# Performance work log

Hardware: AMD Instinct MI355X
Metric: run time of the kernel (lower is better)

Reference implementation:

```python
import jax, jax.numpy as jnp
import numpy as np

B, C, H, W = 4, 512, 96, 96
NH = 8
HD = C // NH
NC = 128
D = 768
L = H * W
EPS = 1e-5  # torch LayerNorm default


def _l2n(x, axis):
    # F.normalize: x / max(||x||, 1e-12)
    return x / jnp.maximum(jnp.linalg.norm(x, axis=axis, keepdims=True), 1e-12)


def _ln2d(x, g, b):
    # LayerNorm2d: normalize over channel dim of (B,C,H,W)
    mu = x.mean(1, keepdims=True)
    var = ((x - mu) ** 2).mean(1, keepdims=True)
    return (x - mu) / jnp.sqrt(var + EPS) * g[None, :, None, None] + b[None, :, None, None]


def _conv1x1(x, w):
    return jnp.einsum('oc,bchw->bohw', w, x)


def setup_inputs() -> dict:
    key = jax.random.key(0)
    ks = jax.random.split(key, 9)
    s = 0.02
    return {
        'img_feats': jax.random.normal(ks[0], (B, C, H, W), jnp.float32),
        'cls_embs': jax.random.normal(ks[1], (NC, D), jnp.float32),
        'cls_logits': jax.random.normal(ks[2], (B, NC), jnp.float32),
        'seg_logits': jax.random.normal(ks[3], (B, 1, H, W), jnp.float32),
        'gamma_g': jnp.ones((D,), jnp.float32), 'beta_g': jnp.zeros((D,), jnp.float32),
        'gamma_f': jnp.ones((C,), jnp.float32), 'beta_f': jnp.zeros((C,), jnp.float32),
        'attn_scale': jnp.ones((NH, 1, 1), jnp.float32),
        'Wg': jax.random.normal(ks[4], (C, D), jnp.float32) * s,
        'Wqkv': jax.random.normal(ks[5], (3 * C, C), jnp.float32) * s,
        'Wo': jax.random.normal(ks[6], (C, C), jnp.float32) * s,
        'bo': jnp.zeros((C,), jnp.float32),
        'gamma_n': jnp.ones((C,), jnp.float32), 'beta_n': jnp.zeros((C,), jnp.float32),
        'W1': jax.random.normal(ks[7], (C, C), jnp.float32) * s, 'b1': jnp.zeros((C,), jnp.float32),
        'W2': jax.random.normal(ks[8], (C, C), jnp.float32) * s, 'b2': jnp.zeros((C,), jnp.float32),
    }


def reference(img_feats, cls_embs, cls_logits, seg_logits, gamma_g, beta_g,
              gamma_f, beta_f, attn_scale, Wg, Wqkv, Wo, bo, gamma_n, beta_n,
              W1, b1, W2, b2):
    xn = _ln2d(img_feats, gamma_f, beta_f)
    # guide LayerNorm over embedding dim
    mu = cls_embs.mean(-1, keepdims=True)
    var = ((cls_embs - mu) ** 2).mean(-1, keepdims=True)
    cn = (cls_embs - mu) / jnp.sqrt(var + EPS) * gamma_g + beta_g
    g = (cn @ Wg.T).reshape(NC, NH, HD)  # nc nh hd

    qkv = _conv1x1(xn, Wqkv).reshape(B, 3, NH, HD, L)
    q, k, v = qkv[:, 0], qkv[:, 1], qkv[:, 2]  # each (B,NH,HD,L)

    # cosine guide map + min-max normalization + softmax-weighted aggregation over classes
    gm = jnp.einsum('nhd,bhdl->bhnl', _l2n(g, -1), _l2n(q, -2))
    gm = gm - gm.min(-1, keepdims=True)
    gm = gm / gm.max(-1, keepdims=True)
    gm = (jax.nn.softmax(gm, axis=2) * gm).sum(2, keepdims=True)  # (B,NH,1,L)

    # auxiliary guide map from cls logits + masked pooling of k
    cls_obj = jnp.einsum('nhd,bn->bhd', g, cls_logits)
    mask = jax.nn.sigmoid(seg_logits)  # (B,1,H,W)
    seg_obj = (mask * k.reshape(B, C, H, W)).sum((2, 3)) / mask.sum((2, 3))  # (B,C)
    obj = _l2n(cls_obj + seg_obj.reshape(B, NH, HD), -1)
    aux = jnp.einsum('bhd,bhdl->bhl', obj, _l2n(k, -2))[:, :, None, :]
    aux = aux - aux.min(-1, keepdims=True)
    aux = aux / aux.max(-1, keepdims=True)
    gm = gm * aux

    v = gm * v
    # channel (transposed) cosine attention: (B,NH,HD,HD)
    attn = jnp.einsum('bhdl,bhel->bhde', _l2n(q, -1), _l2n(k, -1)) * attn_scale
    out = jnp.einsum('bhde,bhel->bhdl', jax.nn.softmax(attn, -1), v).reshape(B, C, H, W)

    x = img_feats + _conv1x1(out, Wo) + bo[None, :, None, None]
    # ConvMlp with pre-norm: LayerNorm2d -> 1x1 conv -> GELU -> 1x1 conv
    fin = _ln2d(x, gamma_n, beta_n)
    h = jax.nn.gelu(_conv1x1(fin, W1) + b1[None, :, None, None], approximate=False)
    return x + _conv1x1(h, W2) + b2[None, :, None, None]
```

## Files before the change

### kernel.cpp

```cpp
#include <hip/hip_runtime.h>
#include <hip/hip_bf16.h>
#include <math.h>

#define BB 4
#define CC 512
#define NHEAD 8
#define HDIM 64
#define NCLS 128
#define DD 768
#define LL 9216
#define BLPIX 36864
#define EPSV 1e-5f
#define GMBLK 144
#define AUXBLK 144
#define LSPLIT 8
#define NLT 72

typedef __hip_bfloat16 bf16;
typedef __attribute__((ext_vector_type(8))) short short8v;
typedef __attribute__((ext_vector_type(4))) short short4v;
typedef __attribute__((ext_vector_type(4))) float f32x4;

__device__ __forceinline__ float bf2f(bf16 v){ return __bfloat162float(v); }
__device__ __forceinline__ bf16 f2bf(float v){ return __float2bfloat16(v); }
__device__ __forceinline__ short bfbits(float v){ bf16 b = __float2bfloat16(v); return *reinterpret_cast<short*>(&b); }
__device__ __forceinline__ float s2f(short s){ bf16 b = *reinterpret_cast<bf16*>(&s); return __bfloat162float(b); }

__global__ __launch_bounds__(256) void wclsg_k(
    const float* __restrict__ wqkv, const float* __restrict__ wo,
    const float* __restrict__ w1, const float* __restrict__ w2,
    bf16* __restrict__ oq, bf16* __restrict__ oo,
    bf16* __restrict__ o1, bf16* __restrict__ o2,
    const float* __restrict__ cls_embs, const float* __restrict__ gamma_g,
    const float* __restrict__ beta_g, const float* __restrict__ Wg,
    float* __restrict__ g, bf16* __restrict__ gnb)
{
  __shared__ __align__(16) float cn[DD];
  __shared__ float red[256];
  __shared__ float gsh[CC];
  __shared__ float nrm[NHEAD];
  int bid = blockIdx.x;
  int tid = threadIdx.x;
  if (bid < 1536){
    int i = bid * 256 + tid;
    int e = i * 4;
    const float* src; bf16* dst; int off;
    if (e < 786432){ src = wqkv; dst = oq; off = e; }
    else if (e < 1048576){ src = wo; dst = oo; off = e - 786432; }
    else if (e < 1310720){ src = w1; dst = o1; off = e - 1048576; }
    else { src = w2; dst = o2; off = e - 1310720; }
    float4 v = *reinterpret_cast<const float4*>(src + off);
    short4v pk;
    pk[0] = bfbits(v.x); pk[1] = bfbits(v.y); pk[2] = bfbits(v.z); pk[3] = bfbits(v.w);
    *(short4v*)&dst[off] = pk;
    return;
  }
  {
    int n = bid - 1536;
    const float* e = cls_embs + (size_t)n * DD;
    float s = 0.f, ss = 0.f;
    for (int i = tid; i < DD; i += 256){ float v = e[i]; s += v; ss += v * v; }
    red[tid] = s; __syncthreads();
    for (int st = 128; st > 0; st >>= 1){ if (tid < st) red[tid] += red[tid + st]; __syncthreads(); }
    float mean = red[0] / DD; __syncthreads();
    red[tid] = ss; __syncthreads();
    for (int st = 128; st > 0; st >>= 1){ if (tid < st) red[tid] += red[tid + st]; __syncthreads(); }
    float var = red[0] / DD - mean * mean;
    float rstd = rsqrtf(var + EPSV);
    __syncthreads();
    for (int i = tid; i < DD; i += 256) cn[i] = (e[i] - mean) * rstd * gamma_g[i] + beta_g[i];
    __syncthreads();
    for (int c = tid; c < CC; c += 256){
      const float* w = Wg + (size_t)c * DD;
      float a = 0.f;
      #pragma unroll 8
      for (int d = 0; d < DD; d++) a += cn[d] * w[d];
      gsh[c] = a;
    }
    __syncthreads();
    if (tid < NHEAD){
      float a = 0.f;
      for (int d = 0; d < HDIM; d++){ float v = gsh[tid * HDIM + d]; a += v * v; }
      nrm[tid] = fmaxf(sqrtf(a), 1e-12f);
    }
    __syncthreads();
    for (int c = tid; c < CC; c += 256){
      g[(size_t)n * CC + c] = gsh[c];
      gnb[(size_t)n * CC + c] = f2bf(gsh[c] / nrm[c >> 6]);
    }
  }
}

__global__ __launch_bounds__(256) void fuse_ln_k(const float* __restrict__ X,
    const float* __restrict__ lng, const float* __restrict__ lnb,
    bf16* __restrict__ xnT){
  __shared__ float sred[2][4][64];
  __shared__ float muS[64], rsS[64];
  __shared__ float t[64][65];
  int p0 = blockIdx.x * 64;
  int b = p0 / LL, l0 = p0 - b * LL;
  int tid = threadIdx.x;
  int cg = tid >> 6, l = tid & 63;
  const float* base = X + (size_t)b * CC * LL + l0 + l;
  float s = 0.f, ss = 0.f;
  for (int c = cg * 128; c < cg * 128 + 128; c++){
    float v = base[(size_t)c * LL];
    s += v; ss += v * v;
  }
  sred[0][cg][l] = s; sred[1][cg][l] = ss;
  __syncthreads();
  if (tid < 64){
    float st = sred[0][0][tid] + sred[0][1][tid] + sred[0][2][tid] + sred[0][3][tid];
    float sst = sred[1][0][tid] + sred[1][1][tid] + sred[1][2][tid] + sred[1][3][tid];
    float m = st * (1.0f / CC);
    float var = sst * (1.0f / CC) - m * m;
    muS[tid] = m; rsS[tid] = rsqrtf(var + EPSV);
  }
  __syncthreads();
  int pr = tid >> 4;
  int cc = (tid & 15) * 4;
  for (int cb = 0; cb < 8; cb++){
    int c0 = cb * 64;
    #pragma unroll
    for (int i = 0; i < 16; i++){
      int idx = i * 256 + tid;
      int cl = idx >> 6, ll2 = idx & 63;
      t[cl][ll2] = X[(size_t)b * CC * LL + (size_t)(c0 + cl) * LL + l0 + ll2];
    }
    __syncthreads();
    #pragma unroll
    for (int i = 0; i < 4; i++){
      int pl = pr + i * 16;
      int p = p0 + pl;
      float m = muS[pl], r = rsS[pl];
      short4v pk;
      #pragma unroll
      for (int e = 0; e < 4; e++){
        int c = c0 + cc + e;
        pk[e] = bfbits((t[cc + e][pl] - m) * r * lng[c] + lnb[c]);
      }
      *(short4v*)&xnT[(size_t)p * CC + c0 + cc] = pk;
    }
    __syncthreads();
  }
}

__global__ void statsred_k(const float2* __restrict__ statp, float* __restrict__ mu, float* __restrict__ rs){
  int p = blockIdx.x * 256 + threadIdx.x;
  if (p >= BLPIX) return;
  float s = 0.f, ss = 0.f;
  #pragma unroll
  for (int part = 0; part < 4; part++){
    float2 v = statp[part * BLPIX + p];
    s += v.x; ss += v.y;
  }
  float m = s * (1.0f / CC);
  float var = ss * (1.0f / CC) - m * m;
  mu[p] = m; rs[p] = rsqrtf(var + EPSV);
}

template<int MODE>
__global__ __launch_bounds__(256, 2) void mgemm_k(
    const bf16* __restrict__ A,
    const bf16* __restrict__ B,
    const float* __restrict__ residf,
    const bf16* __restrict__ residb,
    const float* __restrict__ bias,
    const float* __restrict__ mu, const float* __restrict__ rs,
    const float* __restrict__ lng, const float* __restrict__ lnb,
    float2* __restrict__ statp,
    float* __restrict__ qssp, float* __restrict__ kssp,
    bf16* __restrict__ qTo, float* __restrict__ rqo,
    bf16* __restrict__ ko, bf16* __restrict__ vo,
    bf16* __restrict__ xT_out,
    float* __restrict__ xo,
    bf16* __restrict__ ho,
    const float* __restrict__ gA, const float* __restrict__ clsl, float* __restrict__ clsovO)
{
  __shared__ short Asm[128 * 64];
  __shared__ short Bsm[128 * 64];
  __shared__ float sredf[512];
  int tid = threadIdx.x;
  if (MODE == 0 && blockIdx.x >= 3456){
    int idx = (blockIdx.x - 3456) * 256 + tid;
    int b = idx >> 9, c = idx & 511;
    float a = 0.f;
    for (int n = 0; n < NCLS; n++) a += gA[(size_t)n * CC + c] * clsl[b * NCLS + n];
    clsovO[idx] = a;
    return;
  }
  int lane = tid & 63, wv = tid >> 6;
  int wr = wv >> 1, wc = wv & 1;
  int r15 = lane & 15, g = lane >> 4, h7 = lane & 7;
  int flat, gx, cpx;
  if (MODE == 0){ flat = blockIdx.x; gx = 12; cpx = 432; }
  else { gx = gridDim.x; flat = blockIdx.y * gx + blockIdx.x; cpx = (gx * gridDim.y) >> 3; }
  int swz = (flat & 7) * cpx + (flat >> 3);
  int m0 = (swz % gx) * 128, n0 = (swz / gx) * 128;
  int srow = tid >> 3, skkg = tid & 7;
  int sslot = ((skkg ^ (srow & 7))) * 8;

  f32x4 acc[4][4];
  #pragma unroll
  for (int i = 0; i < 4; i++)
    #pragma unroll
    for (int j = 0; j < 4; j++) acc[i][j] = (f32x4){0.f, 0.f, 0.f, 0.f};

  short8v pa[4], pb[4];
  auto loadAB = [&](int it){
    int k0 = it * 64;
    if (MODE == 2){
      int c0 = k0 + skkg * 8;
      float ga[8], be[8];
      *(float4*)&ga[0] = *(const float4*)&lng[c0];
      *(float4*)&ga[4] = *(const float4*)&lng[c0 + 4];
      *(float4*)&be[0] = *(const float4*)&lnb[c0];
      *(float4*)&be[4] = *(const float4*)&lnb[c0 + 4];
      #pragma unroll
      for (int r = 0; r < 4; r++){
        pa[r] = *reinterpret_cast<const short8v*>(A + (size_t)(m0 + r * 32 + srow) * 512 + c0);
        int rp = n0 + r * 32 + srow;
        float mm = mu[rp], rr = rs[rp];
        short8v rawv = *reinterpret_cast<const short8v*>(B + (size_t)rp * 512 + c0);
        short8v ov;
        #pragma unroll
        for (int e = 0; e < 8; e++){
          float v = (s2f(rawv[e]) - mm) * rr * ga[e] + be[e];
          ov[e] = bfbits(v);
        }
        pb[r] = ov;
      }
    } else {
      #pragma unroll
      for (int r = 0; r < 4; r++){
        pa[r] = *reinterpret_cast<const short8v*>(A + (size_t)(m0 + r * 32 + srow) * 512 + k0 + skkg * 8);
        pb[r] = *reinterpret_cast<const short8v*>(B + (size_t)(n0 + r * 32 + srow) * 512 + k0 + skkg * 8);
      }
    }
  };

  loadAB(0);
  for (int it = 0; it < 8; ++it){
    __syncthreads();
    #pragma unroll
    for (int r = 0; r < 4; r++){
      int row = r * 32 + srow;
      *(short8v*)&Asm[row * 64 + sslot] = pa[r];
      *(short8v*)&Bsm[row * 64 + sslot] = pb[r];
    }
    __syncthreads();
    if (it < 7) loadAB(it + 1);
    #pragma unroll
    for (int s = 0; s < 2; s++){
      int slot = ((s * 4 + g) ^ h7) * 8;
      short8v af[4], bf_[4];
      #pragma unroll
      for (int i = 0; i < 4; i++){
        af[i]  = *(const short8v*)&Asm[(wr * 64 + i * 16 + r15) * 64 + slot];
        bf_[i] = *(const short8v*)&Bsm[(wc * 64 + i * 16 + r15) * 64 + slot];
      }
      #pragma unroll
      for (int i = 0; i < 4; i++)
        #pragma unroll
        for (int j = 0; j < 4; j++){
          if (MODE == 2)
            acc[i][j] = __builtin_amdgcn_mfma_f32_16x16x32_bf16(bf_[i], af[j], acc[i][j], 0, 0, 0);
          else
            acc[i][j] = __builtin_amdgcn_mfma_f32_16x16x32_bf16(af[i], bf_[j], acc[i][j], 0, 0, 0);
        }
    }
  }

  int bIdx = n0 / LL;
  int lbase = n0 - bIdx * LL;
  if (MODE == 0){
    int part = m0 >> 9;
    if (part == 0){
      int chb = m0 + wr * 64;
      #pragma unroll
      for (int i = 0; i < 4; i++)
        #pragma unroll
        for (int j = 0; j < 4; j++){
          int l = lbase + wc * 64 + j * 16 + r15;
          int ch = chb + i * 16 + g * 4;
          short4v pk;
          #pragma unroll
          for (int e = 0; e < 4; e++) pk[e] = bfbits(acc[i][j][e]);
          *(short4v*)&qTo[((size_t)bIdx * LL + l) * CC + ch] = pk;
        }
      int head = chb >> 6;
      int bh = bIdx * 8 + head;
      #pragma unroll
      for (int j = 0; j < 4; j++){
        float ssl = 0.f;
        #pragma unroll
        for (int i = 0; i < 4; i++)
          #pragma unroll
          for (int e = 0; e < 4; e++) ssl += acc[i][j][e] * acc[i][j][e];
        ssl += __shfl_xor(ssl, 16); ssl += __shfl_xor(ssl, 32);
        if (g == 0){
          int l = lbase + wc * 64 + j * 16 + r15;
          rqo[(size_t)bh * LL + l] = 1.0f / fmaxf(sqrtf(ssl), 1e-12f);
        }
      }
      #pragma unroll
      for (int i = 0; i < 4; i++)
        #pragma unroll
        for (int e = 0; e < 4; e++){
          float ssv = acc[i][0][e]*acc[i][0][e] + acc[i][1][e]*acc[i][1][e]
                    + acc[i][2][e]*acc[i][2][e] + acc[i][3][e]*acc[i][3][e];
          #pragma unroll
          for (int msk = 1; msk < 16; msk <<= 1) ssv += __shfl_xor(ssv, msk);
          if (r15 == 0) sredf[wv * 64 + i * 16 + g * 4 + e] = ssv;
        }
      __syncthreads();
      if (tid < 128){
        int wrr = tid >> 6, chL = tid & 63;
        float tot = sredf[(wrr * 2) * 64 + chL] + sredf[(wrr * 2 + 1) * 64 + chL];
        int c = m0 + wrr * 64 + chL;
        int row = bIdx * 512 + c;
        int ltile = lbase >> 7;
        qssp[(size_t)row * NLT + ltile] = tot;
      }
    } else if (part == 1){
      int chb = (m0 & 511) + wr * 64;
      #pragma unroll
      for (int i = 0; i < 4; i++)
        #pragma unroll
        for (int j = 0; j < 4; j++){
          int l = lbase + wc * 64 + j * 16 + r15;
          #pragma unroll
          for (int e = 0; e < 4; e++){
            int ch = chb + i * 16 + g * 4 + e;
            ko[(size_t)bIdx * CC * LL + (size_t)ch * LL + l] = f2bf(acc[i][j][e]);
          }
        }
      #pragma unroll
      for (int i = 0; i < 4; i++)
        #pragma unroll
        for (int e = 0; e < 4; e++){
          float ssv = acc[i][0][e]*acc[i][0][e] + acc[i][1][e]*acc[i][1][e]
                    + acc[i][2][e]*acc[i][2][e] + acc[i][3][e]*acc[i][3][e];
          #pragma unroll
          for (int msk = 1; msk < 16; msk <<= 1) ssv += __shfl_xor(ssv, msk);
          if (r15 == 0) sredf[wv * 64 + i * 16 + g * 4 + e] = ssv;
        }
      __syncthreads();
      if (tid < 128){
        int wrr = tid >> 6, chL = tid & 63;
        float tot = sredf[(wrr * 2) * 64 + chL] + sredf[(wrr * 2 + 1) * 64 + chL];
        int c = (m0 & 511) + wrr * 64 + chL;
        int row = bIdx * 512 + c;
        int ltile = lbase >> 7;
        kssp[(size_t)row * NLT + ltile] = tot;
      }
    } else {
      int chb = (m0 & 511) + wr * 64;
      #pragma unroll
      for (int i = 0; i < 4; i++)
        #pragma unroll
        for (int j = 0; j < 4; j++){
          int l = lbase + wc * 64 + j * 16 + r15;
          int ch = chb + i * 16 + g * 4;
          short4v pk;
          #pragma unroll
          for (int e = 0; e < 4; e++) pk[e] = bfbits(acc[i][j][e]);
          *(short4v*)&vo[((size_t)bIdx * LL + l) * CC + ch] = pk;
        }
    }
  } else if (MODE == 1){
    float sj[4] = {0.f,0.f,0.f,0.f}, ssj[4] = {0.f,0.f,0.f,0.f};
    #pragma unroll
    for (int i = 0; i < 4; i++)
      #pragma unroll
      for (int j = 0; j < 4; j++){
        int l = lbase + wc * 64 + j * 16 + r15;
        int chm = m0 + wr * 64 + i * 16 + g * 4;
        short4v pk;
        #pragma unroll
        for (int e = 0; e < 4; e++){
          int m = chm + e;
          size_t o = (size_t)bIdx * CC * LL + (size_t)m * LL + l;
          float xv = residf[o] + acc[i][j][e] + bias[m];
          pk[e] = bfbits(xv);
          sj[j] += xv; ssj[j] += xv * xv;
        }
        *(short4v*)&xT_out[((size_t)bIdx * LL + l) * CC + chm] = pk;
      }
    #pragma unroll
    for (int j = 0; j < 4; j++){
      sj[j] += __shfl_xor(sj[j], 16); sj[j] += __shfl_xor(sj[j], 32);
      ssj[j] += __shfl_xor(ssj[j], 16); ssj[j] += __shfl_xor(ssj[j], 32);
    }
    if (g == 0){
      #pragma unroll
      for (int j = 0; j < 4; j++){
        sredf[wv * 128 + j * 32 + r15 * 2 + 0] = sj[j];
        sredf[wv * 128 + j * 32 + r15 * 2 + 1] = ssj[j];
      }
    }
    __syncthreads();
    if (tid < 128){
      int wv2 = tid >> 6, lane2 = tid & 63, j2 = lane2 >> 4, r2 = lane2 & 15;
      float s   = sredf[wv2 * 128 + j2 * 32 + r2 * 2 + 0] + sredf[(wv2 + 2) * 128 + j2 * 32 + r2 * 2 + 0];
      float ss2 = sredf[wv2 * 128 + j2 * 32 + r2 * 2 + 1] + sredf[(wv2 + 2) * 128 + j2 * 32 + r2 * 2 + 1];
      int p = n0 + wv2 * 64 + j2 * 16 + r2;
      statp[(m0 >> 7) * BLPIX + p] = make_float2(s, ss2);
    }
  } else if (MODE == 3){
    #pragma unroll
    for (int i = 0; i < 4; i++)
      #pragma unroll
      for (int j = 0; j < 4; j++){
        int l = lbase + wc * 64 + j * 16 + r15;
        int chm = m0 + wr * 64 + i * 16 + g * 4;
        short4v rv = *(const short4v*)&residb[((size_t)bIdx * LL + l) * CC + chm];
        #pragma unroll
        for (int e = 0; e < 4; e++){
          int m = chm + e;
          size_t o = (size_t)bIdx * CC * LL + (size_t)m * LL + l;
          xo[o] = s2f(rv[e]) + acc[i][j][e] + bias[m];
        }
      }
  } else {
    #pragma unroll
    for (int i = 0; i < 4; i++)
      #pragma unroll
      for (int j = 0; j < 4; j++){
        int mm = m0 + wr * 64 + j * 16 + r15;
        float bv = bias[mm];
        #pragma unroll
        for (int e = 0; e < 4; e++){
          int n = n0 + wc * 64 + i * 16 + g * 4 + e;
          float t = acc[i][j][e] + bv;
          float gv = 0.5f * t * (1.0f + erff(t * 0.70710678118654752f));
          ho[(size_t)n * CC + mm] = f2bf(gv);
        }
      }
  }
}

__global__ __launch_bounds__(256) void mega1_k(
    const bf16* __restrict__ qT, const float* __restrict__ rq,
    const bf16* __restrict__ k, const bf16* __restrict__ gnb,
    float* __restrict__ pmin, float* __restrict__ pmax,
    float* __restrict__ part,
    const float* __restrict__ seg, float* __restrict__ seg_num, float* __restrict__ den,
    const float* __restrict__ qssp, const float* __restrict__ kssp,
    float* __restrict__ qn, float* __restrict__ kn)
{
  __shared__ __align__(16) bf16 qs[128 * 68];
  int bid = blockIdx.x;
  int t = threadIdx.x;
  if (bid < 1152){
    int bh = bid & 31, ltg = bid >> 5;
    int b = bh >> 3, h = bh & 7;
    int w = t >> 6, lane = t & 63, r15 = lane & 15, g = lane >> 4;
    short8v ag[2][2];
    #pragma unroll
    for (int i = 0; i < 2; i++)
      #pragma unroll
      for (int kt = 0; kt < 2; kt++)
        ag[i][kt] = *reinterpret_cast<const short8v*>(gnb + (size_t)(w * 32 + i * 16 + r15) * CC + h * 64 + kt * 32 + g * 8);
    for (int sub = 0; sub < 4; sub++){
      int lt = ltg * 4 + sub;
      int l0 = lt * 64;
      const bf16* qTp = qT + ((size_t)(b * LL + l0)) * CC + h * 64;
      short8v bq[4][2];
      float rqv[4];
      #pragma unroll
      for (int j = 0; j < 4; j++){
        #pragma unroll
        for (int kt = 0; kt < 2; kt++)
          bq[j][kt] = *reinterpret_cast<const short8v*>(qTp + (size_t)(j * 16 + r15) * CC + kt * 32 + g * 8);
        rqv[j] = rq[(size_t)bh * LL + l0 + j * 16 + r15];
      }
      f32x4 acc[2][4];
      #pragma unroll
      for (int i = 0; i < 2; i++)
        #pragma unroll
        for (int j = 0; j < 4; j++) acc[i][j] = (f32x4){0.f,0.f,0.f,0.f};
      #pragma unroll
      for (int kt = 0; kt < 2; kt++)
        #pragma unroll
        for (int i = 0; i < 2; i++)
          #pragma unroll
          for (int j = 0; j < 4; j++)
            acc[i][j] = __builtin_amdgcn_mfma_f32_16x16x32_bf16(ag[i][kt], bq[j][kt], acc[i][j], 0, 0, 0);
      #pragma unroll
      for (int i = 0; i < 2; i++)
        #pragma unroll
        for (int e = 0; e < 4; e++){
          float mn = 1e30f, mx = -1e30f;
          #pragma unroll
          for (int j = 0; j < 4; j++){
            float v = acc[i][j][e] * rqv[j];
            mn = fminf(mn, v); mx = fmaxf(mx, v);
          }
          #pragma unroll
          for (int msk = 1; msk < 16; msk <<= 1){
            mn = fminf(mn, __shfl_xor(mn, msk));
            mx = fmaxf(mx, __shfl_xor(mx, msk));
          }
          if (r15 == 0){
            int n = w * 32 + i * 16 + g * 4 + e;
            pmin[((size_t)bh * 128 + n) * GMBLK + lt] = mn;
            pmax[((size_t)bh * 128 + n) * GMBLK + lt] = mx;
          }
        }
    }
    return;
  }
  if (bid < 1408){
    int bid2 = bid - 1152;
    int ls = bid2 & 7, bh = bid2 >> 3;
    int b = bh >> 3, h = bh & 7;
    int w = t >> 6, lane = t & 63, r15 = lane & 15, g = lane >> 4;
    const bf16* kp = k + (size_t)b * CC * LL + (size_t)h * HDIM * LL;
    f32x4 acc4[4];
    #pragma unroll
    for (int j = 0; j < 4; j++) acc4[j] = (f32x4){0.f,0.f,0.f,0.f};
    for (int stg = 0; stg < 9; stg++){
      int lb = ls * 1152 + stg * 128;
      #pragma unroll
      for (int it = 0; it < 8; it++){
        int idx = t + it * 256;
        int row = idx >> 4, c4 = (idx & 15) * 4;
        *(short4v*)&qs[row * 68 + c4] = *(const short4v*)&qT[((size_t)(b * LL + lb + row)) * CC + h * 64 + c4];
      }
      __syncthreads();
      #pragma unroll
      for (int kstep = 0; kstep < 4; kstep++){
        int lloc = kstep * 32 + g * 8;
        short8v aq;
        #pragma unroll
        for (int jj = 0; jj < 8; jj++)
          aq[jj] = *reinterpret_cast<short*>(&qs[(lloc + jj) * 68 + w * 16 + r15]);
        int koff = lb + kstep * 32 + g * 8;
        short8v bk[4];
        #pragma unroll
        for (int j = 0; j < 4; j++) bk[j] = *reinterpret_cast<const short8v*>(kp + (size_t)(j * 16 + r15) * LL + koff);
        #pragma unroll
        for (int j = 0; j < 4; j++)
          acc4[j] = __builtin_amdgcn_mfma_f32_16x16x32_bf16(aq, bk[j], acc4[j], 0, 0, 0);
      }
      __syncthreads();
    }
    #pragma unroll
    for (int j = 0; j < 4; j++)
      #pragma unroll
      for (int e = 0; e < 4; e++){
        int d = w * 16 + g * 4 + e;
        int ee = j * 16 + r15;
        part[((size_t)(bh * LSPLIT + ls)) * 4096 + d * 64 + ee] = acc4[j][e];
      }
    return;
  }
  if (bid < 3456){
    float* red = (float*)qs;
    int bc = bid - 1408;
    int b = bc >> 9;
    const bf16* p = k + (size_t)bc * LL;
    const float* sp = seg + (size_t)b * LL;
    float s = 0.f;
    for (int i = t; i < LL; i += 256){
      float m = 1.0f / (1.0f + expf(-sp[i]));
      s += m * bf2f(p[i]);
    }
    red[t] = s; __syncthreads();
    for (int st = 128; st > 0; st >>= 1){ if (t < st) red[t] += red[t + st]; __syncthreads(); }
    if (t == 0) seg_num[bc] = red[0];
    return;
  }
  if (bid < 3460){
    float* red = (float*)qs;
    int b = bid - 3456;
    const float* sp = seg + (size_t)b * LL;
    float s = 0.f;
    for (int i = t; i < LL; i += 256) s += 1.0f / (1.0f + expf(-sp[i]));
    red[t] = s; __syncthreads();
    for (int st = 128; st > 0; st >>= 1){ if (t < st) red[t] += red[t + st]; __syncthreads(); }
    if (t == 0) den[b] = red[0];
    return;
  }
  {
    int r4 = (bid - 3460) * 4 + (t >> 6);
    int lane = t & 63;
    const float* src = (r4 < 2048) ? qssp : kssp;
    int r = r4 & 2047;
    float s = src[(size_t)r * NLT + lane] + ((lane < 8) ? src[(size_t)r * NLT + 64 + lane] : 0.f);
    #pragma unroll
    for (int m = 1; m < 64; m <<= 1) s += __shfl_xor(s, m);
    if (lane == 0){
      float nv = fmaxf(sqrtf(s), 1e-12f);
      if (r4 < 2048) qn[r] = nv; else kn[r] = nv;
    }
  }
}

__global__ __launch_bounds__(256) void aux_k(const bf16* __restrict__ k,
                      const float* __restrict__ clsov, const float* __restrict__ segn,
                      const float* __restrict__ segd,
                      float* __restrict__ aux,
                      float* __restrict__ pmin, float* __restrict__ pmax){
  __shared__ bf16 ks[64 * 68];
  __shared__ float os[64];
  __shared__ float sspart[4][64], dotpart[4][64];
  int bh = blockIdx.x, lt = blockIdx.y;
  int l0 = lt * 64;
  int t = threadIdx.x;
  int b = bh >> 3, h = bh & 7;
  const bf16* kp = k + (size_t)b * CC * LL + (size_t)h * HDIM * LL + l0;
  #pragma unroll
  for (int i2 = 0; i2 < 4; i2++){
    int idx = t + i2 * 256;
    int d = idx >> 4, lch = (idx & 15) * 4;
    *(short4v*)&ks[d * 68 + lch] = *reinterpret_cast<const short4v*>(kp + (size_t)d * LL + lch);
  }
  if (t < 64){
    float sv = clsov[bh * 64 + t] + segn[bh * 64 + t] / segd[b];
    float ss2 = sv * sv;
    #pragma unroll
    for (int m = 1; m < 64; m <<= 1) ss2 += __shfl_xor(ss2, m);
    os[t] = sv / fmaxf(sqrtf(ss2), 1e-12f);
  }
  __syncthreads();
  {
    int dg = t >> 6, l = t & 63;
    float ssk = 0.f, dk = 0.f;
    #pragma unroll
    for (int dd = 0; dd < 16; dd++){
      float v = bf2f(ks[(dg * 16 + dd) * 68 + l]);
      ssk += v * v; dk += os[dg * 16 + dd] * v;
    }
    sspart[dg][l] = ssk; dotpart[dg][l] = dk;
  }
  __syncthreads();
  if (t < 64){
    float ss = sspart[0][t] + sspart[1][t] + sspart[2][t] + sspart[3][t];
    float dot = dotpart[0][t] + dotpart[1][t] + dotpart[2][t] + dotpart[3][t];
    float av = dot / fmaxf(sqrtf(ss), 1e-12f);
    aux[(size_t)bh * LL + l0 + t] = av;
    float mn = av, mx = av;
    #pragma unroll
    for (int m = 1; m < 64; m <<= 1){
      mn = fminf(mn, __shfl_xor(mn, m));
      mx = fmaxf(mx, __shfl_xor(mx, m));
    }
    if (t == 0){ pmin[bh * AUXBLK + lt] = mn; pmax[bh * AUXBLK + lt] = mx; }
  }
}

__global__ __launch_bounds__(256) void megared_k(
    const float* __restrict__ gpmin, const float* __restrict__ gpmax,
    float* __restrict__ gmin, float* __restrict__ gms,
    const float* __restrict__ apmin, const float* __restrict__ apmax,
    float* __restrict__ amin, float* __restrict__ ams,
    const float* __restrict__ part, const float* __restrict__ qn,
    const float* __restrict__ kn, const float* __restrict__ scale,
    bf16* __restrict__ Pb)
{
  __shared__ float As[64 * 65];
  int bid = blockIdx.x;
  int tid = threadIdx.x;
  if (bid < 1024){
    int row = bid * 4 + (tid >> 6);
    int lane = tid & 63;
    float mn = gpmin[(size_t)row * GMBLK + lane];
    float mx = gpmax[(size_t)row * GMBLK + lane];
    mn = fminf(mn, gpmin[(size_t)row * GMBLK + 64 + lane]);
    mx = fmaxf(mx, gpmax[(size_t)row * GMBLK + 64 + lane]);
    if (lane < 16){
      mn = fminf(mn, gpmin[(size_t)row * GMBLK + 128 + lane]);
      mx = fmaxf(mx, gpmax[(size_t)row * GMBLK + 128 + lane]);
    }
    #pragma unroll
    for (int m = 1; m < 64; m <<= 1){
      mn = fminf(mn, __shfl_xor(mn, m));
      mx = fmaxf(mx, __shfl_xor(mx, m));
    }
    if (lane == 0){ gmin[row] = mn; gms[row] = mx - mn; }
    return;
  }
  if (bid < 1032){
    int bh = (bid - 1024) * 4 + (tid >> 6);
    int lane = tid & 63;
    float mn = apmin[bh * AUXBLK + lane];
    float mx = apmax[bh * AUXBLK + lane];
    mn = fminf(mn, apmin[bh * AUXBLK + 64 + lane]);
    mx = fmaxf(mx, apmax[bh * AUXBLK + 64 + lane]);
    if (lane < 16){
      mn = fminf(mn, apmin[bh * AUXBLK + 128 + lane]);
      mx = fmaxf(mx, apmax[bh * AUXBLK + 128 + lane]);
    }
    #pragma unroll
    for (int m = 1; m < 64; m <<= 1){
      mn = fminf(mn, __shfl_xor(mn, m));
      mx = fmaxf(mx, __shfl_xor(mx, m));
    }
    if (lane == 0){ amin[bh] = mn; ams[bh] = mx - mn; }
    return;
  }
  {
    int bh = bid - 1032;
    int h = bh & 7;
    #pragma unroll
    for (int i = 0; i < 16; i++){
      int cell = tid + i * 256;
      int d = cell >> 6, e = cell & 63;
      float s = 0.f;
      #pragma unroll
      for (int ls = 0; ls < LSPLIT; ls++) s += part[((size_t)(bh * LSPLIT + ls)) * 4096 + cell];
      As[d * 65 + e] = s * scale[h] / (qn[bh * 64 + d] * kn[bh * 64 + e]);
    }
    __syncthreads();
    if (tid < 64){
      int d = tid;
      float mx = -1e30f;
      for (int e = 0; e < 64; e++) mx = fmaxf(mx, As[d * 65 + e]);
      float sum = 0.f;
      for (int e = 0; e < 64; e++){ float ev = expf(As[d * 65 + e] - mx); As[d * 65 + e] = ev; sum += ev; }
      float inv = 1.0f / sum;
      for (int e = 0; e < 64; e++) Pb[(size_t)bh * 4096 + d * 64 + e] = f2bf(As[d * 65 + e] * inv);
    }
  }
}

__global__ __launch_bounds__(256) void pv_k(const bf16* __restrict__ qT, const float* __restrict__ rq,
      const bf16* __restrict__ gnb,
      const float* __restrict__ aux,
      const float* __restrict__ gmin, const float* __restrict__ gms,
      const float* __restrict__ amin, const float* __restrict__ ams,
      const bf16* __restrict__ Pb, const bf16* __restrict__ vT, bf16* __restrict__ outT){
  __shared__ float gminS[128], rgmsS[128];
  __shared__ float separt[4][64], setpart[4][64];
  __shared__ float wl[64];
  int bh = blockIdx.x, lt = blockIdx.y;
  int l0 = lt * 64;
  int t = threadIdx.x;
  int b = bh >> 3, h = bh & 7;
  int w = t >> 6, lane = t & 63, r15 = lane & 15, g = lane >> 4;
  if (t < 128){ gminS[t] = gmin[bh * 128 + t]; rgmsS[t] = 1.0f / gms[bh * 128 + t]; }
  short8v ag[2][2];
  #pragma unroll
  for (int i = 0; i < 2; i++)
    #pragma unroll
    for (int kt = 0; kt < 2; kt++)
      ag[i][kt] = *reinterpret_cast<const short8v*>(gnb + (size_t)(w * 32 + i * 16 + r15) * CC + h * 64 + kt * 32 + g * 8);
  const bf16* qTp = qT + ((size_t)(b * LL + l0)) * CC + h * 64;
  short8v bq[4][2];
  float rqv[4];
  #pragma unroll
  for (int j = 0; j < 4; j++){
    #pragma unroll
    for (int kt = 0; kt < 2; kt++)
      bq[j][kt] = *reinterpret_cast<const short8v*>(qTp + (size_t)(j * 16 + r15) * CC + kt * 32 + g * 8);
    rqv[j] = rq[(size_t)bh * LL + l0 + j * 16 + r15];
  }
  f32x4 acc[2][4];
  #pragma unroll
  for (int i = 0; i < 2; i++)
    #pragma unroll
    for (int j = 0; j < 4; j++) acc[i][j] = (f32x4){0.f,0.f,0.f,0.f};
  #pragma unroll
  for (int kt = 0; kt < 2; kt++)
    #pragma unroll
    for (int i = 0; i < 2; i++)
      #pragma unroll
      for (int j = 0; j < 4; j++)
        acc[i][j] = __builtin_amdgcn_mfma_f32_16x16x32_bf16(ag[i][kt], bq[j][kt], acc[i][j], 0, 0, 0);
  __syncthreads();
  float seL[4] = {0.f,0.f,0.f,0.f}, setL[4] = {0.f,0.f,0.f,0.f};
  #pragma unroll
  for (int i = 0; i < 2; i++)
    #pragma unroll
    for (int j = 0; j < 4; j++)
      #pragma unroll
      for (int e = 0; e < 4; e++){
        int n = w * 32 + i * 16 + g * 4 + e;
        float tt = (acc[i][j][e] * rqv[j] - gminS[n]) * rgmsS[n];
        float ee = __expf(tt);
        seL[j] += ee; setL[j] += ee * tt;
      }
  #pragma unroll
  for (int j = 0; j < 4; j++){
    seL[j] += __shfl_xor(seL[j], 16); seL[j] += __shfl_xor(seL[j], 32);
    setL[j] += __shfl_xor(setL[j], 16); setL[j] += __shfl_xor(setL[j], 32);
  }
  if (g == 0){
    #pragma unroll
    for (int j = 0; j < 4; j++){ separt[w][j * 16 + r15] = seL[j]; setpart[w][j * 16 + r15] = setL[j]; }
  }
  __syncthreads();
  if (t < 64){
    float se = separt[0][t] + separt[1][t] + separt[2][t] + separt[3][t];
    float st = setpart[0][t] + setpart[1][t] + setpart[2][t] + setpart[3][t];
    float gmred = st / se;
    float auxn = (aux[(size_t)bh * LL + l0 + t] - amin[bh]) / ams[bh];
    wl[t] = gmred * auxn;
  }
  __syncthreads();
  short8v ap[4][2];
  #pragma unroll
  for (int i = 0; i < 4; i++)
    #pragma unroll
    for (int kt = 0; kt < 2; kt++)
      ap[i][kt] = *reinterpret_cast<const short8v*>(Pb + (size_t)bh * 4096 + (i * 16 + r15) * 64 + kt * 32 + g * 8);
  const bf16* vrow = vT + ((size_t)b * LL + l0 + w * 16 + r15) * CC + h * 64;
  short8v bv[2];
  #pragma unroll
  for (int kt = 0; kt < 2; kt++) bv[kt] = *reinterpret_cast<const short8v*>(vrow + kt * 32 + g * 8);
  f32x4 oacc[4];
  #pragma unroll
  for (int i = 0; i < 4; i++) oacc[i] = (f32x4){0.f,0.f,0.f,0.f};
  #pragma unroll
  for (int kt = 0; kt < 2; kt++)
    #pragma unroll
    for (int i = 0; i < 4; i++)
      oacc[i] = __builtin_amdgcn_mfma_f32_16x16x32_bf16(ap[i][kt], bv[kt], oacc[i], 0, 0, 0);
  float wlv = wl[w * 16 + r15];
  bf16* orow = outT + ((size_t)b * LL + l0 + w * 16 + r15) * CC + h * 64;
  #pragma unroll
  for (int i = 0; i < 4; i++){
    short4v pk;
    #pragma unroll
    for (int e = 0; e < 4; e++) pk[e] = bfbits(oacc[i][e] * wlv);
    *(short4v*)&orow[i * 16 + g * 4] = pk;
  }
}

extern "C" void kernel_launch(void* const* d_in, const int* in_sizes, int n_in,
                              void* d_out, int out_size, void* d_ws, size_t ws_size,
                              hipStream_t stream){
  const float* img        = (const float*)d_in[0];
  const float* cls_embs   = (const float*)d_in[1];
  const float* cls_logits = (const float*)d_in[2];
  const float* seg        = (const float*)d_in[3];
  const float* gamma_g    = (const float*)d_in[4];
  const float* beta_g     = (const float*)d_in[5];
  const float* gamma_f    = (const float*)d_in[6];
  const float* beta_f     = (const float*)d_in[7];
  const float* attn_scale = (const float*)d_in[8];
  const float* Wg         = (const float*)d_in[9];
  const float* Wqkv       = (const float*)d_in[10];
  const float* Wo         = (const float*)d_in[11];
  const float* bo         = (const float*)d_in[12];
  const float* gamma_n    = (const float*)d_in[13];
  const float* beta_n     = (const float*)d_in[14];
  const float* W1         = (const float*)d_in[15];
  const float* b1         = (const float*)d_in[16];
  const float* W2         = (const float*)d_in[17];
  const float* b2         = (const float*)d_in[18];
  float* outp = (float*)d_out;
  (void)in_sizes; (void)n_in; (void)out_size;

  char* wsb = (char*)d_ws;
  size_t off = 0;
  auto alloc = [&](size_t bytes)->char*{
    char* p = wsb + off;
    off += (bytes + 255) & ~(size_t)255;
    return p;
  };
  float* mu1   = (float*)alloc((size_t)BLPIX * 4);
  float* rs1   = (float*)alloc((size_t)BLPIX * 4);
  float2* statp= (float2*)alloc((size_t)4 * BLPIX * 8);
  float* qssp  = (float*)alloc((size_t)2048 * NLT * 4);
  float* kssp  = (float*)alloc((size_t)2048 * NLT * 4);
  float* qn    = (float*)alloc(2048 * 4);
  float* kn    = (float*)alloc(2048 * 4);
  float* rqb   = (float*)alloc((size_t)32 * LL * 4);
  float* gbuf  = (float*)alloc((size_t)NCLS * CC * 4);
  bf16*  gnbb  = (bf16*)alloc((size_t)NCLS * CC * 2);
  float* clsov = (float*)alloc(2048 * 4);
  float* segn  = (float*)alloc(2048 * 4);
  float* segd  = (float*)alloc(256);
  float* gminp = (float*)alloc((size_t)32 * 128 * GMBLK * 4);
  float* gmaxp = (float*)alloc((size_t)32 * 128 * GMBLK * 4);
  float* gminv = (float*)alloc(4096 * 4);
  float* gmsv  = (float*)alloc(4096 * 4);
  float* auxv  = (float*)alloc((size_t)32 * LL * 4);
  float* apmin = (float*)alloc(32 * AUXBLK * 4);
  float* apmax = (float*)alloc(32 * AUXBLK * 4);
  float* aminv = (float*)alloc(256);
  float* amsv  = (float*)alloc(256);
  bf16*  Pb    = (bf16*)alloc((size_t)32 * 4096 * 2);
  float* apart = (float*)alloc((size_t)32 * LSPLIT * 4096 * 4);
  bf16* qb    = (bf16*)alloc((size_t)BB * CC * LL * 2);
  bf16* kb    = (bf16*)alloc((size_t)BB * CC * LL * 2);
  bf16* wqkvb = (bf16*)alloc((size_t)1536 * 512 * 2);
  bf16* wob   = (bf16*)alloc((size_t)512 * 512 * 2);
  bf16* w1b   = (bf16*)alloc((size_t)512 * 512 * 2);
  bf16* w2b   = (bf16*)alloc((size_t)512 * 512 * 2);
  bf16* vT  = (bf16*)d_out;
  bf16* xnT = (bf16*)((char*)d_out + (size_t)BB * CC * LL * 2);
  bf16* qTb = qb;
  bf16* outT = kb;
  bf16* xT   = qb;
  bf16* hbT  = kb;
  if (off > ws_size) return;

  wclsg_k<<<1664, 256, 0, stream>>>(Wqkv, Wo, W1, W2, wqkvb, wob, w1b, w2b,
      cls_embs, gamma_g, beta_g, Wg, gbuf, gnbb);
  fuse_ln_k<<<576, 256, 0, stream>>>(img, gamma_f, beta_f, xnT);
  mgemm_k<0><<<3464, 256, 0, stream>>>(wqkvb, xnT, nullptr, nullptr, nullptr,
      nullptr, nullptr, nullptr, nullptr, nullptr, qssp, kssp,
      qTb, rqb, kb, vT, nullptr, nullptr, nullptr,
      gbuf, cls_logits, clsov);
  mega1_k<<<4484, 256, 0, stream>>>(qTb, rqb, kb, gnbb, gminp, gmaxp, apart,
      seg, segn, segd, qssp, kssp, qn, kn);
  aux_k<<<dim3(32, 144), 256, 0, stream>>>(kb, clsov, segn, segd, auxv, apmin, apmax);
  megared_k<<<1064, 256, 0, stream>>>(gminp, gmaxp, gminv, gmsv,
      apmin, apmax, aminv, amsv,
      apart, qn, kn, attn_scale, Pb);
  pv_k<<<dim3(32, GMBLK), 256, 0, stream>>>(qTb, rqb, gnbb, auxv, gminv, gmsv, aminv, amsv, Pb, vT, outT);
  mgemm_k<1><<<dim3(4, 288), 256, 0, stream>>>(wob, outT, img, nullptr, bo,
      nullptr, nullptr, nullptr, nullptr, statp, nullptr, nullptr,
      nullptr, nullptr, nullptr, nullptr, xT, nullptr, nullptr,
      nullptr, nullptr, nullptr);
  statsred_k<<<144, 256, 0, stream>>>(statp, mu1, rs1);
  mgemm_k<2><<<dim3(4, 288), 256, 0, stream>>>(w1b, xT, nullptr, nullptr, b1,
      mu1, rs1, gamma_n, beta_n, nullptr, nullptr, nullptr,
      nullptr, nullptr, nullptr, nullptr, nullptr, nullptr, hbT,
      nullptr, nullptr, nullptr);
  mgemm_k<3><<<dim3(4, 288), 256, 0, stream>>>(w2b, hbT, nullptr, xT, b2,
      nullptr, nullptr, nullptr, nullptr, nullptr, nullptr, nullptr,
      nullptr, nullptr, nullptr, nullptr, nullptr, outp, nullptr,
      nullptr, nullptr, nullptr);
}
```

Baseline: 468.0 us.

## Use direct global-to-LDS loads in GEMMs and fuse LayerNorm stats reduction

For GEMM modes 0, 1 and 3, the register-staged, XOR-swizzled LDS fill is replaced with global_load_lds 16-byte direct loads into an unswizzled tile, dropping the register prefetch. The separate stats-reduction kernel is removed, and mode 2 now reduces the per-pixel mean and rstd partials into shared memory at block start. This saves a launch and the VGPR staging traffic. In exchange the loads are no longer overlapped with compute (single buffer), and the unswizzled LDS layout may cause bank conflicts on the fragment reads.

```diff
diff --git a/kernel.cpp b/kernel.cpp
--- a/kernel.cpp
+++ b/kernel.cpp
@@ -25,6 +25,10 @@
 __device__ __forceinline__ bf16 f2bf(float v){ return __float2bfloat16(v); }
 __device__ __forceinline__ short bfbits(float v){ bf16 b = __float2bfloat16(v); return *reinterpret_cast<short*>(&b); }
 __device__ __forceinline__ float s2f(short s){ bf16 b = *reinterpret_cast<bf16*>(&s); return __bfloat162float(b); }
+__device__ __forceinline__ void gload16(const bf16* g, short* l){
+  __builtin_amdgcn_global_load_lds((const __attribute__((address_space(1))) void*)g,
+                                   (__attribute__((address_space(3))) void*)l, 16, 0, 0);
+}
 
 __global__ __launch_bounds__(256) void wclsg_k(
     const float* __restrict__ wqkv, const float* __restrict__ wo,
@@ -145,20 +149,6 @@
   }
 }
 
-__global__ void statsred_k(const float2* __restrict__ statp, float* __restrict__ mu, float* __restrict__ rs){
-  int p = blockIdx.x * 256 + threadIdx.x;
-  if (p >= BLPIX) return;
-  float s = 0.f, ss = 0.f;
-  #pragma unroll
-  for (int part = 0; part < 4; part++){
-    float2 v = statp[part * BLPIX + p];
-    s += v.x; ss += v.y;
-  }
-  float m = s * (1.0f / CC);
-  float var = ss * (1.0f / CC) - m * m;
-  mu[p] = m; rs[p] = rsqrtf(var + EPSV);
-}
-
 template<int MODE>
 __global__ __launch_bounds__(256, 2) void mgemm_k(
     const bf16* __restrict__ A,
@@ -166,7 +156,6 @@
     const float* __restrict__ residf,
     const bf16* __restrict__ residb,
     const float* __restrict__ bias,
-    const float* __restrict__ mu, const float* __restrict__ rs,
     const float* __restrict__ lng, const float* __restrict__ lnb,
     float2* __restrict__ statp,
     float* __restrict__ qssp, float* __restrict__ kssp,
@@ -191,14 +180,13 @@
   }
   int lane = tid & 63, wv = tid >> 6;
   int wr = wv >> 1, wc = wv & 1;
-  int r15 = lane & 15, g = lane >> 4, h7 = lane & 7;
+  int r15 = lane & 15, g = lane >> 4;
   int flat, gx, cpx;
   if (MODE == 0){ flat = blockIdx.x; gx = 12; cpx = 432; }
   else { gx = gridDim.x; flat = blockIdx.y * gx + blockIdx.x; cpx = (gx * gridDim.y) >> 3; }
   int swz = (flat & 7) * cpx + (flat >> 3);
   int m0 = (swz % gx) * 128, n0 = (swz / gx) * 128;
   int srow = tid >> 3, skkg = tid & 7;
-  int sslot = ((skkg ^ (srow & 7))) * 8;
 
   f32x4 acc[4][4];
   #pragma unroll
@@ -206,10 +194,46 @@
     #pragma unroll
     for (int j = 0; j < 4; j++) acc[i][j] = (f32x4){0.f, 0.f, 0.f, 0.f};
 
-  short8v pa[4], pb[4];
-  auto loadAB = [&](int it){
-    int k0 = it * 64;
-    if (MODE == 2){
+  auto compute = [&](){
+    #pragma unroll
+    for (int s = 0; s < 2; s++){
+      int slot = s * 32 + g * 8;
+      short8v af[4], bf_[4];
+      #pragma unroll
+      for (int i = 0; i < 4; i++){
+        af[i]  = *(const short8v*)&Asm[(wr * 64 + i * 16 + r15) * 64 + slot];
+        bf_[i] = *(const short8v*)&Bsm[(wc * 64 + i * 16 + r15) * 64 + slot];
+      }
+      #pragma unroll
+      for (int i = 0; i < 4; i++)
+        #pragma unroll
+        for (int j = 0; j < 4; j++){
+          if (MODE == 2)
+            acc[i][j] = __builtin_amdgcn_mfma_f32_16x16x32_bf16(bf_[i], af[j], acc[i][j], 0, 0, 0);
+          else
+            acc[i][j] = __builtin_amdgcn_mfma_f32_16x16x32_bf16(af[i], bf_[j], acc[i][j], 0, 0, 0);
+        }
+    }
+  };
+
+  if (MODE == 2){
+    if (tid < 128){
+      int p = n0 + tid;
+      float s = 0.f, ss2 = 0.f;
+      #pragma unroll
+      for (int part = 0; part < 4; part++){
+        float2 v = statp[part * BLPIX + p];
+        s += v.x; ss2 += v.y;
+      }
+      float m = s * (1.0f / CC);
+      float var = ss2 * (1.0f / CC) - m * m;
+      sredf[tid] = m;
+      sredf[128 + tid] = rsqrtf(var + EPSV);
+    }
+    __syncthreads();
+    short8v pa[4], pb[4];
+    auto loadAB = [&](int it){
+      int k0 = it * 64;
       int c0 = k0 + skkg * 8;
       float ga[8], be[8];
       *(float4*)&ga[0] = *(const float4*)&lng[c0];
@@ -219,9 +243,9 @@
       #pragma unroll
       for (int r = 0; r < 4; r++){
         pa[r] = *reinterpret_cast<const short8v*>(A + (size_t)(m0 + r * 32 + srow) * 512 + c0);
-        int rp = n0 + r * 32 + srow;
-        float mm = mu[rp], rr = rs[rp];
-        short8v rawv = *reinterpret_cast<const short8v*>(B + (size_t)rp * 512 + c0);
+        int rl = r * 32 + srow;
+        float mm = sredf[rl], rr = sredf[128 + rl];
+        short8v rawv = *reinterpret_cast<const short8v*>(B + (size_t)(n0 + rl) * 512 + c0);
         short8v ov;
         #pragma unroll
         for (int e = 0; e < 8; e++){
@@ -230,44 +254,33 @@
         }
         pb[r] = ov;
       }
-    } else {
+    };
+    loadAB(0);
+    for (int it = 0; it < 8; ++it){
+      __syncthreads();
       #pragma unroll
       for (int r = 0; r < 4; r++){
-        pa[r] = *reinterpret_cast<const short8v*>(A + (size_t)(m0 + r * 32 + srow) * 512 + k0 + skkg * 8);
-        pb[r] = *reinterpret_cast<const short8v*>(B + (size_t)(n0 + r * 32 + srow) * 512 + k0 + skkg * 8);
-      }
-    }
-  };
-
-  loadAB(0);
-  for (int it = 0; it < 8; ++it){
-    __syncthreads();
-    #pragma unroll
-    for (int r = 0; r < 4; r++){
-      int row = r * 32 + srow;
-      *(short8v*)&Asm[row * 64 + sslot] = pa[r];
-      *(short8v*)&Bsm[row * 64 + sslot] = pb[r];
-    }
-    __syncthreads();
-    if (it < 7) loadAB(it + 1);
-    #pragma unroll
-    for (int s = 0; s < 2; s++){
-      int slot = ((s * 4 + g) ^ h7) * 8;
-      short8v af[4], bf_[4];
-      #pragma unroll
-      for (int i = 0; i < 4; i++){
-        af[i]  = *(const short8v*)&Asm[(wr * 64 + i * 16 + r15) * 64 + slot];
-        bf_[i] = *(const short8v*)&Bsm[(wc * 64 + i * 16 + r15) * 64 + slot];
-      }
-      #pragma unroll
-      for (int i = 0; i < 4; i++)
-        #pragma unroll
-        for (int j = 0; j < 4; j++){
-          if (MODE == 2)
-            acc[i][j] = __builtin_amdgcn_mfma_f32_16x16x32_bf16(bf_[i], af[j], acc[i][j], 0, 0, 0);
-          else
-            acc[i][j] = __builtin_amdgcn_mfma_f32_16x16x32_bf16(af[i], bf_[j], acc[i][j], 0, 0, 0);
-        }
+        int row = r * 32 + srow;
+        *(short8v*)&Asm[row * 64 + skkg * 8] = pa[r];
+        *(short8v*)&Bsm[row * 64 + skkg * 8] = pb[r];
+      }
+      __syncthreads();
+      if (it < 7) loadAB(it + 1);
+      compute();
+    }
+  } else {
+    for (int it = 0; it < 8; ++it){
+      if (it) __syncthreads();
+      int k0 = it * 64;
+      #pragma unroll
+      for (int r = 0; r < 4; r++){
+        gload16(A + (size_t)(m0 + wv * 8 + (lane >> 3) + r * 32) * 512 + k0 + (lane & 7) * 8,
+                Asm + ((wv * 64 + r * 256) << 3));
+        gload16(B + (size_t)(n0 + wv * 8 + (lane >> 3) + r * 32) * 512 + k0 + (lane & 7) * 8,
+                Bsm + ((wv * 64 + r * 256) << 3));
+      }
+      __syncthreads();
+      compute();
     }
   }
 
@@ -861,8 +874,6 @@
     off += (bytes + 255) & ~(size_t)255;
     return p;
   };
-  float* mu1   = (float*)alloc((size_t)BLPIX * 4);
-  float* rs1   = (float*)alloc((size_t)BLPIX * 4);
   float2* statp= (float2*)alloc((size_t)4 * BLPIX * 8);
   float* qssp  = (float*)alloc((size_t)2048 * NLT * 4);
   float* kssp  = (float*)alloc((size_t)2048 * NLT * 4);
@@ -903,7 +914,7 @@
       cls_embs, gamma_g, beta_g, Wg, gbuf, gnbb);
   fuse_ln_k<<<576, 256, 0, stream>>>(img, gamma_f, beta_f, xnT);
   mgemm_k<0><<<3464, 256, 0, stream>>>(wqkvb, xnT, nullptr, nullptr, nullptr,
-      nullptr, nullptr, nullptr, nullptr, nullptr, qssp, kssp,
+      nullptr, nullptr, nullptr, qssp, kssp,
       qTb, rqb, kb, vT, nullptr, nullptr, nullptr,
       gbuf, cls_logits, clsov);
   mega1_k<<<4484, 256, 0, stream>>>(qTb, rqb, kb, gnbb, gminp, gmaxp, apart,
@@ -914,16 +925,15 @@
       apart, qn, kn, attn_scale, Pb);
   pv_k<<<dim3(32, GMBLK), 256, 0, stream>>>(qTb, rqb, gnbb, auxv, gminv, gmsv, aminv, amsv, Pb, vT, outT);
   mgemm_k<1><<<dim3(4, 288), 256, 0, stream>>>(wob, outT, img, nullptr, bo,
-      nullptr, nullptr, nullptr, nullptr, statp, nullptr, nullptr,
+      nullptr, nullptr, statp, nullptr, nullptr,
       nullptr, nullptr, nullptr, nullptr, xT, nullptr, nullptr,
       nullptr, nullptr, nullptr);
-  statsred_k<<<144, 256, 0, stream>>>(statp, mu1, rs1);
   mgemm_k<2><<<dim3(4, 288), 256, 0, stream>>>(w1b, xT, nullptr, nullptr, b1,
-      mu1, rs1, gamma_n, beta_n, nullptr, nullptr, nullptr,
+      gamma_n, beta_n, statp, nullptr, nullptr,
       nullptr, nullptr, nullptr, nullptr, nullptr, nullptr, hbT,
       nullptr, nullptr, nullptr);
   mgemm_k<3><<<dim3(4, 288), 256, 0, stream>>>(w2b, hbT, nullptr, xT, b2,
-      nullptr, nullptr, nullptr, nullptr, nullptr, nullptr, nullptr,
+      nullptr, nullptr, nullptr, nullptr, nullptr,
       nullptr, nullptr, nullptr, nullptr, nullptr, outp, nullptr,
       nullptr, nullptr, nullptr);
 }
```

Result: no change. 472.8 us (+1.0%).
